# Kernel tuning notes

Measured on AMD Instinct MI355X. Metric: run time of the kernel, lower is better.

Reference implementation:

```python
import jax, jax.numpy as jnp
import numpy as np

B, S, D = 4, 2048, 512
E, K = 8, 2
MH = 4 * D      # resmlp mlp hidden
EH = 2 * D      # expert hidden
EPS = 1e-5


def setup_inputs() -> dict:
    key = jax.random.key(0)
    ks = jax.random.split(key, 16)
    s = 0.02
    return {
        "x": jax.random.normal(ks[0], (B, S, D), dtype=jnp.float32),
        "ln1_g": jnp.ones((D,), jnp.float32), "ln1_b": jnp.zeros((D,), jnp.float32),
        "w1": jax.random.normal(ks[1], (D, MH), jnp.float32) * s,
        "b1": jnp.zeros((MH,), jnp.float32),
        "w2": jax.random.normal(ks[2], (MH, D), jnp.float32) * s,
        "b2": jnp.zeros((D,), jnp.float32),
        "ln2_g": jnp.ones((D,), jnp.float32), "ln2_b": jnp.zeros((D,), jnp.float32),
        "wr": jax.random.normal(ks[3], (E, D), jnp.float32) * s,
        "ew1": jax.random.normal(ks[4], (E, D, EH), jnp.float32) * s,
        "eb1": jnp.zeros((E, EH), jnp.float32),
        "ew2": jax.random.normal(ks[5], (E, EH, D), jnp.float32) * s,
        "eb2": jnp.zeros((E, D), jnp.float32),
        "lnf_g": jnp.ones((D,), jnp.float32), "lnf_b": jnp.zeros((D,), jnp.float32),
    }


def _ln(z, g, b):
    m = z.mean(-1, keepdims=True)
    v = ((z - m) ** 2).mean(-1, keepdims=True)
    return (z - m) * jax.lax.rsqrt(v + EPS) * g + b


def reference(x, ln1_g, ln1_b, w1, b1, w2, b2, ln2_g, ln2_b,
              wr, ew1, eb1, ew2, eb2, lnf_g, lnf_b):
    # ---- ResidualMLPBlock (eval mode: dropout is identity) ----
    h = _ln(x, ln1_g, ln1_b)
    h = jax.nn.gelu(h @ w1 + b1, approximate=False) @ w2 + b2
    x = x + h
    x = _ln(x, ln2_g, ln2_b) + x
    # ---- MoE (eval: no jitter noise, aux_loss = 0) ----
    xf = x.reshape(-1, D)              # [N, D], N = B*S
    n = xf.shape[0]
    probs = jax.nn.softmax(xf @ wr.T, axis=-1)          # [N, E]
    topv, topi = jax.lax.top_k(probs, K)                # [N, K]
    topv = topv / topv.sum(-1, keepdims=True)
    # dense per-token gate per expert: sum over k of renormalized prob where idx==j
    gates = jnp.zeros((n, E), xf.dtype).at[jnp.arange(n)[:, None], topi].add(topv)
    # per-expert MLP over all tokens (masked scatter-combine via gates)
    he = jax.nn.gelu(jnp.einsum("nd,edh->enh", xf, ew1) + eb1[:, None, :],
                     approximate=False)                 # [E, N, 2D]
    ye = jnp.einsum("enh,ehd->end", he, ew2) + eb2[:, None, :]  # [E, N, D]
    out = jnp.einsum("ne,end->nd", gates, ye).reshape(B, S, D)
    # ---- final LayerNorm ----
    out = _ln(out, lnf_g, lnf_b)
    aux_loss = jnp.zeros((), x.dtype)  # eval mode
    return out, aux_loss
```

## Files before the change

kernel.cpp:

```cpp
#include <hip/hip_runtime.h>

#define NTOK 8192
#define DIM  512
#define MHID 2048
#define EHID 1024
#define NEXP 8
#define RBLK 64

using half_t = _Float16;
typedef _Float16 f16x8 __attribute__((ext_vector_type(8)));
typedef float    f32x16 __attribute__((ext_vector_type(16)));

#define MFMA32(a, b, c) __builtin_amdgcn_mfma_f32_32x32x16_f16((a), (b), (c), 0, 0, 0)

typedef const __attribute__((address_space(1))) void* gas_ptr;
typedef __attribute__((address_space(3))) void*       las_ptr;
__device__ __forceinline__ void gl16(const void* g, void* l) {
    __builtin_amdgcn_global_load_lds((gas_ptr)g, (las_ptr)l, 16, 0, 0);
}

__device__ __forceinline__ float gelu_exact(float v) {
    return 0.5f * v * (1.0f + erff(v * 0.70710678118654752f));
}

__device__ __forceinline__ float block_sum4(float v, float* red, int tid) {
#pragma unroll
    for (int off = 32; off; off >>= 1) v += __shfl_down(v, off);
    if ((tid & 63) == 0) red[tid >> 6] = v;
    __syncthreads();
    float r = red[0] + red[1] + red[2] + red[3];
    __syncthreads();
    return r;
}

__global__ __launch_bounds__(256) void ln1_split_kernel(
    const float* __restrict__ x, const float* __restrict__ g, const float* __restrict__ b,
    half_t* __restrict__ xh, half_t* __restrict__ xl, int* __restrict__ cnt)
{
    const int row = blockIdx.x, tid = threadIdx.x;
    if (row == 0) cnt[tid] = 0;
    __shared__ float red[4];
    const size_t base = (size_t)row * DIM;
    float2 v = reinterpret_cast<const float2*>(x + base)[tid];
    float mean = block_sum4(v.x + v.y, red, tid) * (1.0f / DIM);
    float d0 = v.x - mean, d1 = v.y - mean;
    float var = block_sum4(d0 * d0 + d1 * d1, red, tid) * (1.0f / DIM);
    float rstd = rsqrtf(var + 1e-5f);
    int d = tid * 2;
    float y0 = d0 * rstd * g[d]     + b[d];
    float y1 = d1 * rstd * g[d + 1] + b[d + 1];
    half_t h0 = (half_t)y0, h1 = (half_t)y1;
    xh[base + d] = h0;  xh[base + d + 1] = h1;
    xl[base + d]     = (half_t)(y0 - (float)h0);
    xl[base + d + 1] = (half_t)(y1 - (float)h1);
}

__global__ __launch_bounds__(256) void resid_ln2_kernel(
    const float* __restrict__ x, float* __restrict__ p0, const float* __restrict__ p1,
    const float* __restrict__ b2,
    const float* __restrict__ g, const float* __restrict__ b,
    half_t* __restrict__ x3h)
{
    const int row = blockIdx.x, tid = threadIdx.x;
    __shared__ float red[4];
    const size_t base = (size_t)row * DIM;
    float2 xv = reinterpret_cast<const float2*>(x + base)[tid];
    float2 h0 = reinterpret_cast<float2*>(p0 + base)[tid];
    float2 h1 = reinterpret_cast<const float2*>(p1 + base)[tid];
    float2 bb = reinterpret_cast<const float2*>(b2)[tid];
    float z0 = xv.x + h0.x + h1.x + bb.x, z1 = xv.y + h0.y + h1.y + bb.y;
    float mean = block_sum4(z0 + z1, red, tid) * (1.0f / DIM);
    float d0 = z0 - mean, d1 = z1 - mean;
    float var = block_sum4(d0 * d0 + d1 * d1, red, tid) * (1.0f / DIM);
    float rstd = rsqrtf(var + 1e-5f);
    int d = tid * 2;
    float y0 = d0 * rstd * g[d]     + b[d]     + z0;
    float y1 = d1 * rstd * g[d + 1] + b[d + 1] + z1;
    float2 o; o.x = y0; o.y = y1;
    reinterpret_cast<float2*>(p0 + base)[tid] = o;
    x3h[base + d]     = (half_t)y0;
    x3h[base + d + 1] = (half_t)y1;
}

__global__ void transpose_all_kernel(
    const float* __restrict__ w1, const float* __restrict__ w2,
    const float* __restrict__ ew1, const float* __restrict__ ew2,
    half_t* __restrict__ w1t_h, half_t* __restrict__ w1t_l,
    half_t* __restrict__ w2t_h, half_t* __restrict__ w2t_l,
    half_t* __restrict__ ew1t, half_t* __restrict__ ew2t)
{
    int bb = blockIdx.x;
    const float* in; half_t* oh; half_t* ol = (half_t*)0;
    int R, C, cx, cy; size_t mo = 0;
    if (bb < 1024)      { in = w1;  oh = w1t_h; ol = w1t_l; R = 512;  C = 2048; cx = bb & 63; cy = bb >> 6; }
    else if (bb < 2048) { bb -= 1024; in = w2;  oh = w2t_h; ol = w2t_l; R = 2048; C = 512; cx = bb & 15; cy = bb >> 4; }
    else if (bb < 6144) { bb -= 2048; int e = bb >> 9, r = bb & 511;
                          in = ew1; oh = ew1t; R = 512;  C = 1024; mo = (size_t)e * R * C; cx = r & 31; cy = r >> 5; }
    else                { bb -= 6144; int e = bb >> 9, r = bb & 511;
                          in = ew2; oh = ew2t; R = 1024; C = 512;  mo = (size_t)e * R * C; cx = r & 15; cy = r >> 4; }
    __shared__ float t[32][33];
    const int c0 = cx * 32, r0 = cy * 32;
    const int tx = threadIdx.x, ty = threadIdx.y;
    for (int i = ty; i < 32; i += 8) t[i][tx] = in[mo + (size_t)(r0 + i) * C + c0 + tx];
    __syncthreads();
    for (int i = ty; i < 32; i += 8) {
        float v = t[tx][i];
        size_t o = mo + (size_t)(c0 + i) * R + r0 + tx;
        half_t h = (half_t)v;
        oh[o] = h;
        if (ol) ol[o] = (half_t)(v - (float)h);
    }
}

template <int EPI, int NREP>
__global__ __launch_bounds__(512, 2) void gemm8_kernel(
    const half_t* __restrict__ A0, const half_t* __restrict__ A1,
    const half_t* __restrict__ B0, const half_t* __restrict__ B1,
    const float* __restrict__ bias,
    float* __restrict__ Cf0, float* __restrict__ Cf1,
    half_t* __restrict__ Ch, half_t* __restrict__ Cl,
    int Nc, int K, int Ktile)
{
    constexpr int BN    = NREP * 128;
    constexpr int LOADS = 4 + 2 * NREP;
    constexpr int TOT   = 16384 + NREP * 8192;
    __shared__ __align__(16) half_t lds[2 * TOT];

    const int m0 = blockIdx.x * 256, n0 = blockIdx.y * BN;
    const int kbeg = blockIdx.z * Ktile;
    float* Cf = blockIdx.z ? Cf1 : Cf0;
    const int tid = threadIdx.x;
    const int lane = tid & 63, wid = tid >> 6;
    const int wr = wid >> 2, wc = wid & 3;
    const int l31 = lane & 31, l5 = lane >> 5;

    const half_t* gsrc[LOADS];
    {
        const half_t* A0p = A0 + (size_t)m0 * K + kbeg;
        const half_t* A1p = A1 + (size_t)m0 * K + kbeg;
        const half_t* B0p = B0 + (size_t)n0 * K + kbeg;
        const half_t* B1p = B1 + (size_t)n0 * K + kbeg;
#pragma unroll
        for (int i = 0; i < LOADS; i++) {
            int c = tid + 512 * i;
            const half_t* base; int cm;
            if (c < 1024)                  { base = A0p; cm = c; }
            else if (c < 2048)             { base = A1p; cm = c - 1024; }
            else if (c < 2048 + NREP * 512){ base = B0p; cm = c - 2048; }
            else                           { base = B1p; cm = c - 2048 - NREP * 512; }
            int r = cm >> 2, ss = (cm & 3) ^ ((r >> 1) & 3);
            gsrc[i] = base + (size_t)r * K + ss * 8;
        }
    }

    int oa[4][2], ob[NREP][2];
#pragma unroll
    for (int m = 0; m < 4; m++)
#pragma unroll
        for (int kh = 0; kh < 2; kh++) {
            int ra = wr * 128 + m * 32 + l31;
            oa[m][kh] = ra * 32 + (((l5 + 2 * kh) ^ ((ra >> 1) & 3)) << 3);
        }
#pragma unroll
    for (int n = 0; n < NREP; n++)
#pragma unroll
        for (int kh = 0; kh < 2; kh++) {
            int rb = wc * (NREP * 32) + n * 32 + l31;
            ob[n][kh] = rb * 32 + (((l5 + 2 * kh) ^ ((rb >> 1) & 3)) << 3);
        }

    f32x16 acc[4][NREP];
#pragma unroll
    for (int m = 0; m < 4; m++)
#pragma unroll
        for (int n = 0; n < NREP; n++)
#pragma unroll
            for (int q = 0; q < 16; q++) acc[m][n][q] = 0.f;

    auto stage = [&](int bsel, int kof) {
#pragma unroll
        for (int i = 0; i < LOADS; i++)
            gl16(gsrc[i] + kof, &lds[bsel * TOT + (tid + 512 * i) * 8]);
    };
    auto compute = [&](int p) {
        const half_t* buf = &lds[p ? TOT : 0];
        __builtin_amdgcn_s_setprio(1);
#pragma unroll
        for (int kh = 0; kh < 2; kh++) {
            f16x8 ah[4], al[4], bh[NREP], bl[NREP];
#pragma unroll
            for (int m = 0; m < 4; m++) {
                ah[m] = *(const f16x8*)(buf + oa[m][kh]);
                al[m] = *(const f16x8*)(buf + 8192 + oa[m][kh]);
            }
#pragma unroll
            for (int n = 0; n < NREP; n++) {
                bh[n] = *(const f16x8*)(buf + 16384 + ob[n][kh]);
                bl[n] = *(const f16x8*)(buf + 16384 + BN * 32 + ob[n][kh]);
            }
#pragma unroll
            for (int m = 0; m < 4; m++)
#pragma unroll
                for (int n = 0; n < NREP; n++) {
                    acc[m][n] = MFMA32(ah[m], bh[n], acc[m][n]);
                    acc[m][n] = MFMA32(al[m], bh[n], acc[m][n]);
                    acc[m][n] = MFMA32(ah[m], bl[n], acc[m][n]);
                }
        }
        __builtin_amdgcn_s_setprio(0);
    };

    const int nsteps = Ktile / 32;
    stage(0, 0);
#pragma unroll 1
    for (int s = 0; s < nsteps - 1; ++s) {
        stage((s + 1) & 1, (s + 1) * 32);
        if constexpr (NREP == 2) asm volatile("s_waitcnt vmcnt(8)" ::: "memory");
        else                     asm volatile("s_waitcnt vmcnt(6)" ::: "memory");
        __builtin_amdgcn_s_barrier();
        compute(s & 1);
        __builtin_amdgcn_s_barrier();
    }
    asm volatile("s_waitcnt vmcnt(0)" ::: "memory");
    __builtin_amdgcn_s_barrier();
    compute((nsteps - 1) & 1);

    const int er = 4 * l5;
#pragma unroll
    for (int m = 0; m < 4; m++)
#pragma unroll
        for (int n = 0; n < NREP; n++) {
            int cc = n0 + wc * (NREP * 32) + n * 32 + l31;
            float bv = (EPI == 1) ? bias[cc] : 0.f;
#pragma unroll
            for (int reg = 0; reg < 16; reg++) {
                int rr = m0 + wr * 128 + m * 32 + er + 8 * (reg >> 2) + (reg & 3);
                float v = acc[m][n][reg] + bv;
                size_t o = (size_t)rr * Nc + cc;
                if (EPI == 1) {
                    float ge = gelu_exact(v);
                    half_t h = (half_t)ge;
                    Ch[o] = h;
                    Cl[o] = (half_t)(ge - (float)h);
                } else {
                    Cf[o] = v;
                }
            }
        }
}

__global__ __launch_bounds__(256) void router_kernel(
    const float* __restrict__ x3, const float* __restrict__ wrm,
    int* __restrict__ cnt, int* __restrict__ aid, float* __restrict__ gate)
{
    __shared__ float wl[NEXP][DIM];
    __shared__ int   texp[RBLK * 2];
    __shared__ float tgate[RBLK * 2];
    __shared__ int   lslot[RBLK * 2];
    __shared__ int   lcnt[NEXP], lbase[NEXP];
    const int tid = threadIdx.x;
    for (int i = tid; i < NEXP * DIM / 4; i += 256)
        reinterpret_cast<float4*>(&wl[0][0])[i] = reinterpret_cast<const float4*>(wrm)[i];
    if (tid < NEXP) lcnt[tid] = 0;
    __syncthreads();
    const int w = tid >> 6, lane = tid & 63;
#pragma unroll 1
    for (int t = 0; t < RBLK / 4; ++t) {
        const int lt = w * (RBLK / 4) + t;
        const int token = blockIdx.x * RBLK + lt;
        const float* xr = x3 + (size_t)token * DIM;
        float a[NEXP];
#pragma unroll
        for (int e = 0; e < NEXP; e++) a[e] = 0.f;
#pragma unroll
        for (int d0 = 0; d0 < DIM; d0 += 64) {
            float xv = xr[d0 + lane];
#pragma unroll
            for (int e = 0; e < NEXP; e++) a[e] += xv * wl[e][d0 + lane];
        }
#pragma unroll
        for (int e = 0; e < NEXP; e++)
#pragma unroll
            for (int off = 32; off; off >>= 1) a[e] += __shfl_xor(a[e], off);
        if (lane == 0) {
            int i1 = 0; float v1 = a[0];
#pragma unroll
            for (int e = 1; e < NEXP; e++) if (a[e] > v1) { v1 = a[e]; i1 = e; }
            int i2 = -1; float v2 = -3.4e38f;
#pragma unroll
            for (int e = 0; e < NEXP; e++) if (e != i1 && a[e] > v2) { v2 = a[e]; i2 = e; }
            float e2 = expf(v2 - v1);
            float g1 = 1.0f / (1.0f + e2);
            texp[lt * 2]      = i1; tgate[lt * 2]      = g1;
            texp[lt * 2 + 1]  = i2; tgate[lt * 2 + 1]  = 1.0f - g1;
        }
    }
    __syncthreads();
    if (tid < RBLK * 2) lslot[tid] = atomicAdd(&lcnt[texp[tid]], 1);
    __syncthreads();
    if (tid < NEXP) lbase[tid] = atomicAdd(&cnt[tid * 32], lcnt[tid]);
    __syncthreads();
    if (tid < RBLK * 2) {
        const int e = texp[tid];
        const int asg = blockIdx.x * (RBLK * 2) + tid;
        aid[e * NTOK + lbase[e] + lslot[tid]] = asg;
        gate[asg] = tgate[tid];
    }
}

__global__ __launch_bounds__(256) void egemm1_kernel(
    const half_t* __restrict__ X,
    const half_t* __restrict__ W,
    const float* __restrict__ eb1,
    const int* __restrict__ cnt, const int* __restrict__ aid,
    half_t* __restrict__ He)
{
    const int bid = blockIdx.x;
    const int e = bid >> 9, rem = bid & 511;
    const int mt = rem >> 3, nt = rem & 7;
    const int ne = cnt[e * 32];
    if (mt * 128 >= ne) return;
    __shared__ __align__(16) half_t As[2][128 * 32];
    __shared__ __align__(16) half_t Bs[2][128 * 32];
    __shared__ int rowmap[128];
    const int tid = threadIdx.x;
    if (tid < 128) {
        int slot = mt * 128 + tid;
        rowmap[tid] = (slot < ne) ? aid[e * NTOK + slot] : -1;
    }
    __syncthreads();
    const int lane = tid & 63, wid = tid >> 6;
    const int wr = wid >> 1, wc = wid & 1;
    const int c0 = tid, c1 = tid + 256;
    const int r0 = c0 >> 2, s0 = (c0 & 3) ^ ((r0 >> 1) & 3);
    const int r1 = c1 >> 2, s1 = (c1 & 3) ^ ((r1 >> 1) & 3);
    const int a0r = rowmap[r0], a1r = rowmap[r1];
    const half_t* pa0 = X + (size_t)(a0r >= 0 ? (a0r >> 1) : 0) * DIM + s0 * 8;
    const half_t* pa1 = X + (size_t)(a1r >= 0 ? (a1r >> 1) : 0) * DIM + s1 * 8;
    const half_t* pb0 = W + (size_t)e * EHID * DIM + (size_t)(nt * 128 + r0) * DIM + s0 * 8;
    const half_t* pb1 = W + (size_t)e * EHID * DIM + (size_t)(nt * 128 + r1) * DIM + s1 * 8;

    const int l31 = lane & 31, l5 = lane >> 5;
    int oa[2][2], ob[2][2];
#pragma unroll
    for (int i = 0; i < 2; i++)
#pragma unroll
        for (int kh = 0; kh < 2; kh++) {
            int ra = wr * 64 + i * 32 + l31;
            oa[i][kh] = ra * 32 + (((l5 + kh * 2) ^ ((ra >> 1) & 3)) << 3);
            int rb = wc * 64 + i * 32 + l31;
            ob[i][kh] = rb * 32 + (((l5 + kh * 2) ^ ((rb >> 1) & 3)) << 3);
        }
    f32x16 acc[2][2];
#pragma unroll
    for (int i = 0; i < 2; i++)
#pragma unroll
        for (int j = 0; j < 2; j++)
#pragma unroll
            for (int q = 0; q < 16; q++) acc[i][j][q] = 0.f;

    auto stage = [&](int bsel, int k0) {
        gl16(pa0 + k0, &As[bsel][c0 * 8]);
        gl16(pa1 + k0, &As[bsel][c1 * 8]);
        gl16(pb0 + k0, &Bs[bsel][c0 * 8]);
        gl16(pb1 + k0, &Bs[bsel][c1 * 8]);
    };
    auto compute = [&](int bsel) {
#pragma unroll
        for (int kh = 0; kh < 2; kh++) {
            f16x8 a0 = *(const f16x8*)(&As[bsel][0] + oa[0][kh]);
            f16x8 a1 = *(const f16x8*)(&As[bsel][0] + oa[1][kh]);
            f16x8 b0 = *(const f16x8*)(&Bs[bsel][0] + ob[0][kh]);
            f16x8 b1 = *(const f16x8*)(&Bs[bsel][0] + ob[1][kh]);
            acc[0][0] = MFMA32(a0, b0, acc[0][0]);
            acc[0][1] = MFMA32(a0, b1, acc[0][1]);
            acc[1][0] = MFMA32(a1, b0, acc[1][0]);
            acc[1][1] = MFMA32(a1, b1, acc[1][1]);
        }
    };

    stage(0, 0);
#pragma unroll 1
    for (int k0 = 0; k0 < DIM; k0 += 64) {
        __syncthreads();
        if (k0 + 32 < DIM) stage(1, k0 + 32);
        compute(0);
        __syncthreads();
        if (k0 + 64 < DIM) stage(0, k0 + 64);
        compute(1);
    }
    const int er = 4 * l5;
#pragma unroll
    for (int i = 0; i < 2; i++)
#pragma unroll
        for (int reg = 0; reg < 16; reg++) {
            int rloc = wr * 64 + i * 32 + er + 8 * (reg >> 2) + (reg & 3);
            int a = rowmap[rloc];
            if (a >= 0) {
#pragma unroll
                for (int j = 0; j < 2; j++) {
                    int cc = nt * 128 + wc * 64 + j * 32 + l31;
                    float v = acc[i][j][reg] + eb1[e * EHID + cc];
                    He[(size_t)a * EHID + cc] = (half_t)gelu_exact(v);
                }
            }
        }
}

__global__ __launch_bounds__(256) void egemm2_kernel(
    const half_t* __restrict__ Hin,
    const half_t* __restrict__ W,
    const float* __restrict__ eb2,
    const int* __restrict__ cnt, const int* __restrict__ aid,
    const float* __restrict__ gate,
    float* __restrict__ Ye)
{
    const int bid = blockIdx.x;
    const int e = bid >> 8, rem = bid & 255;
    const int mt = rem >> 2, nt = rem & 3;
    const int ne = cnt[e * 32];
    if (mt * 128 >= ne) return;
    __shared__ __align__(16) half_t As[2][128 * 32];
    __shared__ __align__(16) half_t Bs[2][128 * 32];
    __shared__ int rowmap[128];
    const int tid = threadIdx.x;
    if (tid < 128) {
        int slot = mt * 128 + tid;
        rowmap[tid] = (slot < ne) ? aid[e * NTOK + slot] : -1;
    }
    __syncthreads();
    const int lane = tid & 63, wid = tid >> 6;
    const int wr = wid >> 1, wc = wid & 1;
    const int l31 = lane & 31, l5 = lane >> 5;
    const int c0 = tid, c1 = tid + 256;
    const int r0 = c0 >> 2, s0 = (c0 & 3) ^ ((r0 >> 1) & 3);
    const int r1 = c1 >> 2, s1 = (c1 & 3) ^ ((r1 >> 1) & 3);
    const int a0r = rowmap[r0], a1r = rowmap[r1];
    const half_t* pa0 = Hin + (size_t)(a0r >= 0 ? a0r : 0) * EHID + s0 * 8;
    const half_t* pa1 = Hin + (size_t)(a1r >= 0 ? a1r : 0) * EHID + s1 * 8;
    const half_t* pb0 = W + (size_t)e * DIM * EHID + (size_t)(nt * 128 + r0) * EHID + s0 * 8;
    const half_t* pb1 = W + (size_t)e * DIM * EHID + (size_t)(nt * 128 + r1) * EHID + s1 * 8;

    int oa[2][2], ob[2][2];
#pragma unroll
    for (int i = 0; i < 2; i++)
#pragma unroll
        for (int kh = 0; kh < 2; kh++) {
            int ra = wr * 64 + i * 32 + l31;
            oa[i][kh] = ra * 32 + (((l5 + kh * 2) ^ ((ra >> 1) & 3)) << 3);
            int rb = wc * 64 + i * 32 + l31;
            ob[i][kh] = rb * 32 + (((l5 + kh * 2) ^ ((rb >> 1) & 3)) << 3);
        }
    f32x16 acc[2][2];
#pragma unroll
    for (int i = 0; i < 2; i++)
#pragma unroll
        for (int j = 0; j < 2; j++)
#pragma unroll
            for (int q = 0; q < 16; q++) acc[i][j][q] = 0.f;

    auto stage = [&](int bsel, int k0) {
        gl16(pa0 + k0, &As[bsel][c0 * 8]);
        gl16(pa1 + k0, &As[bsel][c1 * 8]);
        gl16(pb0 + k0, &Bs[bsel][c0 * 8]);
        gl16(pb1 + k0, &Bs[bsel][c1 * 8]);
    };
    auto compute = [&](int bsel) {
#pragma unroll
        for (int kh = 0; kh < 2; kh++) {
            f16x8 a0 = *(const f16x8*)(&As[bsel][0] + oa[0][kh]);
            f16x8 a1 = *(const f16x8*)(&As[bsel][0] + oa[1][kh]);
            f16x8 b0 = *(const f16x8*)(&Bs[bsel][0] + ob[0][kh]);
            f16x8 b1 = *(const f16x8*)(&Bs[bsel][0] + ob[1][kh]);
            acc[0][0] = MFMA32(a0, b0, acc[0][0]);
            acc[0][1] = MFMA32(a0, b1, acc[0][1]);
            acc[1][0] = MFMA32(a1, b0, acc[1][0]);
            acc[1][1] = MFMA32(a1, b1, acc[1][1]);
        }
    };

    stage(0, 0);
#pragma unroll 1
    for (int k0 = 0; k0 < EHID; k0 += 64) {
        __syncthreads();
        if (k0 + 32 < EHID) stage(1, k0 + 32);
        compute(0);
        __syncthreads();
        if (k0 + 64 < EHID) stage(0, k0 + 64);
        compute(1);
    }
    const int er = 4 * l5;
#pragma unroll
    for (int i = 0; i < 2; i++)
#pragma unroll
        for (int reg = 0; reg < 16; reg++) {
            int rloc = wr * 64 + i * 32 + er + 8 * (reg >> 2) + (reg & 3);
            int a = rowmap[rloc];
            if (a >= 0) {
                float gv = gate[a];
#pragma unroll
                for (int j = 0; j < 2; j++) {
                    int cc = nt * 128 + wc * 64 + j * 32 + l31;
                    float v = (acc[i][j][reg] + eb2[e * DIM + cc]) * gv;
                    Ye[(size_t)a * DIM + cc] = v;
                }
            }
        }
}

__global__ __launch_bounds__(256) void combine_lnf_kernel(
    const float* __restrict__ Ye, const float* __restrict__ g, const float* __restrict__ b,
    float* __restrict__ out)
{
    const int t = blockIdx.x, tid = threadIdx.x;
    __shared__ float red[4];
    float2 y0 = reinterpret_cast<const float2*>(Ye + (size_t)(2 * t) * DIM)[tid];
    float2 y1 = reinterpret_cast<const float2*>(Ye + (size_t)(2 * t + 1) * DIM)[tid];
    float z0 = y0.x + y1.x, z1 = y0.y + y1.y;
    float mean = block_sum4(z0 + z1, red, tid) * (1.0f / DIM);
    float d0 = z0 - mean, d1 = z1 - mean;
    float var = block_sum4(d0 * d0 + d1 * d1, red, tid) * (1.0f / DIM);
    float rstd = rsqrtf(var + 1e-5f);
    int d = tid * 2;
    out[(size_t)t * DIM + d]     = d0 * rstd * g[d]     + b[d];
    out[(size_t)t * DIM + d + 1] = d1 * rstd * g[d + 1] + b[d + 1];
    if (t == 0 && tid == 0) out[(size_t)NTOK * DIM] = 0.f;
}

extern "C" void kernel_launch(void* const* d_in, const int* in_sizes, int n_in,
                              void* d_out, int out_size, void* d_ws, size_t ws_size,
                              hipStream_t stream)
{
    (void)in_sizes; (void)n_in; (void)out_size; (void)ws_size;
    const float* x    = (const float*)d_in[0];
    const float* ln1g = (const float*)d_in[1];
    const float* ln1b = (const float*)d_in[2];
    const float* w1   = (const float*)d_in[3];
    const float* b1   = (const float*)d_in[4];
    const float* w2   = (const float*)d_in[5];
    const float* b2   = (const float*)d_in[6];
    const float* ln2g = (const float*)d_in[7];
    const float* ln2b = (const float*)d_in[8];
    const float* wrm  = (const float*)d_in[9];
    const float* ew1  = (const float*)d_in[10];
    const float* eb1  = (const float*)d_in[11];
    const float* ew2  = (const float*)d_in[12];
    const float* eb2  = (const float*)d_in[13];
    const float* lnfg = (const float*)d_in[14];
    const float* lnfb = (const float*)d_in[15];
    float* out = (float*)d_out;

    char* w = (char*)d_ws;
    size_t off = 0;
    auto take = [&](size_t bytes) {
        char* p = w + off;
        off += bytes;
        off = (off + 255) & ~(size_t)255;
        return p;
    };
    half_t* xh_h  = (half_t*)take((size_t)NTOK * DIM * 2);
    half_t* xh_l  = (half_t*)take((size_t)NTOK * DIM * 2);
    half_t* w1t_h = (half_t*)take((size_t)DIM * MHID * 2);
    half_t* w1t_l = (half_t*)take((size_t)DIM * MHID * 2);
    half_t* w2t_h = (half_t*)take((size_t)MHID * DIM * 2);
    half_t* w2t_l = (half_t*)take((size_t)MHID * DIM * 2);
    char*   big   = take((size_t)NTOK * MHID * 2 * 2);
    half_t* a1h   = (half_t*)big;
    half_t* a1l   = (half_t*)(big + (size_t)NTOK * MHID * 2);
    half_t* heh   = (half_t*)big;
    float*  yef   = (float*)(big + (size_t)NTOK * MHID * 2);
    float*  x3f   = (float*)take((size_t)NTOK * DIM * 4);
    half_t* x3h   = (half_t*)take((size_t)NTOK * DIM * 2);
    half_t* ew1t  = (half_t*)take((size_t)NEXP * DIM * EHID * 2);
    half_t* ew2t  = (half_t*)take((size_t)NEXP * EHID * DIM * 2);
    int*    cnt   = (int*)take(1024);
    int*    aid   = (int*)take((size_t)NEXP * NTOK * 4);
    float*  gate  = (float*)take((size_t)NTOK * 2 * 4);

    float* p0 = x3f;
    float* p1 = (float*)xh_h;

    ln1_split_kernel<<<NTOK, 256, 0, stream>>>(x, ln1g, ln1b, xh_h, xh_l, cnt);
    transpose_all_kernel<<<10240, dim3(32, 8), 0, stream>>>(
        w1, w2, ew1, ew2, w1t_h, w1t_l, w2t_h, w2t_l, ew1t, ew2t);
    gemm8_kernel<1, 2><<<dim3(NTOK / 256, MHID / 256, 1), 512, 0, stream>>>(
        xh_h, xh_l, w1t_h, w1t_l, b1, (float*)0, (float*)0, a1h, a1l, MHID, DIM, DIM);
    gemm8_kernel<0, 1><<<dim3(NTOK / 256, DIM / 128, 2), 512, 0, stream>>>(
        a1h, a1l, w2t_h, w2t_l, (const float*)0, p0, p1, (half_t*)0, (half_t*)0, DIM, MHID, MHID / 2);
    resid_ln2_kernel<<<NTOK, 256, 0, stream>>>(x, p0, p1, b2, ln2g, ln2b, x3h);
    router_kernel<<<NTOK / RBLK, 256, 0, stream>>>(x3f, wrm, cnt, aid, gate);
    egemm1_kernel<<<NEXP * (NTOK / 128) * (EHID / 128), 256, 0, stream>>>(x3h, ew1t, eb1, cnt, aid, heh);
    egemm2_kernel<<<NEXP * (NTOK / 128) * (DIM / 128), 256, 0, stream>>>(heh, ew2t, eb2, cnt, aid, gate, yef);
    combine_lnf_kernel<<<NTOK, 256, 0, stream>>>(yef, lnfg, lnfb, out);
}
```

Measured before the change: 309.1 us.

## Merge expert GEMMs into one templated kernel with 256-row tiles and waitcnt pipelining

Replaces the two expert GEMM kernels with a single templated kernel that uses 512-thread blocks and 256x128 tiles, so each weight tile is reused across twice as many routed rows. The k-loop now issues the next stage's loads before computing and waits with explicit vmcnt and raw barriers instead of two __syncthreads per pair of steps. It also raises wave priority around the MFMA section. The aim is less weight traffic and better overlap of loads with compute. The cost is more padding waste in each expert's last row tile and a higher LDS footprint per block.

```diff
diff --git a/kernel.cpp b/kernel.cpp
--- a/kernel.cpp
+++ b/kernel.cpp
@@ -308,201 +308,132 @@
     }
 }
 
-__global__ __launch_bounds__(256) void egemm1_kernel(
-    const half_t* __restrict__ X,
+template <int EG, int KDIM, int AROWSHIFT>
+__global__ __launch_bounds__(512, 2) void egemm8_kernel(
+    const half_t* __restrict__ Ain,
     const half_t* __restrict__ W,
-    const float* __restrict__ eb1,
+    const float* __restrict__ ebias,
     const int* __restrict__ cnt, const int* __restrict__ aid,
-    half_t* __restrict__ He)
-{
+    const float* __restrict__ gate,
+    half_t* __restrict__ Oh,
+    float* __restrict__ Of,
+    int Nc)
+{
+    const int ntPerE = Nc / 128;
     const int bid = blockIdx.x;
-    const int e = bid >> 9, rem = bid & 511;
-    const int mt = rem >> 3, nt = rem & 7;
-    const int ne = cnt[e * 32];
-    if (mt * 128 >= ne) return;
-    __shared__ __align__(16) half_t As[2][128 * 32];
-    __shared__ __align__(16) half_t Bs[2][128 * 32];
-    __shared__ int rowmap[128];
+    const int e   = bid / (32 * ntPerE);
+    const int rem = bid % (32 * ntPerE);
+    const int mt  = rem / ntPerE, nt = rem % ntPerE;
+    const int ne  = cnt[e * 32];
+    if (mt * 256 >= ne) return;
+
+    constexpr int TOT = 8192 + 4096;
+    __shared__ __align__(16) half_t lds[2 * TOT];
+    __shared__ int rowmap[256];
     const int tid = threadIdx.x;
-    if (tid < 128) {
-        int slot = mt * 128 + tid;
-        rowmap[tid] = (slot < ne) ? aid[e * NTOK + slot] : -1;
-    }
-    __syncthreads();
+    {
+        int slot = mt * 256 + tid;
+        if (tid < 256) rowmap[tid] = (slot < ne) ? aid[e * NTOK + slot] : -1;
+    }
+    __syncthreads();
+
     const int lane = tid & 63, wid = tid >> 6;
     const int wr = wid >> 1, wc = wid & 1;
-    const int c0 = tid, c1 = tid + 256;
-    const int r0 = c0 >> 2, s0 = (c0 & 3) ^ ((r0 >> 1) & 3);
-    const int r1 = c1 >> 2, s1 = (c1 & 3) ^ ((r1 >> 1) & 3);
-    const int a0r = rowmap[r0], a1r = rowmap[r1];
-    const half_t* pa0 = X + (size_t)(a0r >= 0 ? (a0r >> 1) : 0) * DIM + s0 * 8;
-    const half_t* pa1 = X + (size_t)(a1r >= 0 ? (a1r >> 1) : 0) * DIM + s1 * 8;
-    const half_t* pb0 = W + (size_t)e * EHID * DIM + (size_t)(nt * 128 + r0) * DIM + s0 * 8;
-    const half_t* pb1 = W + (size_t)e * EHID * DIM + (size_t)(nt * 128 + r1) * DIM + s1 * 8;
-
     const int l31 = lane & 31, l5 = lane >> 5;
+
+    const half_t* gsrc[3];
+    const half_t* Wb = W + (size_t)e * Nc * KDIM;
+#pragma unroll
+    for (int i = 0; i < 3; i++) {
+        int c = tid + 512 * i;
+        if (c < 1024) {
+            int r = c >> 2, ss = (c & 3) ^ ((r >> 1) & 3);
+            int a = rowmap[r];
+            gsrc[i] = Ain + (size_t)(a >= 0 ? (a >> AROWSHIFT) : 0) * KDIM + ss * 8;
+        } else {
+            int cb = c - 1024;
+            int r = cb >> 2, ss = (cb & 3) ^ ((r >> 1) & 3);
+            gsrc[i] = Wb + (size_t)(nt * 128 + r) * KDIM + ss * 8;
+        }
+    }
+
     int oa[2][2], ob[2][2];
 #pragma unroll
-    for (int i = 0; i < 2; i++)
+    for (int m = 0; m < 2; m++)
 #pragma unroll
         for (int kh = 0; kh < 2; kh++) {
-            int ra = wr * 64 + i * 32 + l31;
-            oa[i][kh] = ra * 32 + (((l5 + kh * 2) ^ ((ra >> 1) & 3)) << 3);
-            int rb = wc * 64 + i * 32 + l31;
-            ob[i][kh] = rb * 32 + (((l5 + kh * 2) ^ ((rb >> 1) & 3)) << 3);
-        }
+            int ra = wr * 64 + m * 32 + l31;
+            oa[m][kh] = ra * 32 + (((l5 + 2 * kh) ^ ((ra >> 1) & 3)) << 3);
+        }
+#pragma unroll
+    for (int n = 0; n < 2; n++)
+#pragma unroll
+        for (int kh = 0; kh < 2; kh++) {
+            int rb = wc * 64 + n * 32 + l31;
+            ob[n][kh] = 8192 + rb * 32 + (((l5 + 2 * kh) ^ ((rb >> 1) & 3)) << 3);
+        }
+
     f32x16 acc[2][2];
 #pragma unroll
-    for (int i = 0; i < 2; i++)
-#pragma unroll
-        for (int j = 0; j < 2; j++)
-#pragma unroll
-            for (int q = 0; q < 16; q++) acc[i][j][q] = 0.f;
-
-    auto stage = [&](int bsel, int k0) {
-        gl16(pa0 + k0, &As[bsel][c0 * 8]);
-        gl16(pa1 + k0, &As[bsel][c1 * 8]);
-        gl16(pb0 + k0, &Bs[bsel][c0 * 8]);
-        gl16(pb1 + k0, &Bs[bsel][c1 * 8]);
+    for (int m = 0; m < 2; m++)
+#pragma unroll
+        for (int n = 0; n < 2; n++)
+#pragma unroll
+            for (int q = 0; q < 16; q++) acc[m][n][q] = 0.f;
+
+    auto stage = [&](int bsel, int kof) {
+#pragma unroll
+        for (int i = 0; i < 3; i++)
+            gl16(gsrc[i] + kof, &lds[bsel * TOT + (tid + 512 * i) * 8]);
     };
-    auto compute = [&](int bsel) {
+    auto compute = [&](int p) {
+        const half_t* buf = &lds[p ? TOT : 0];
+        __builtin_amdgcn_s_setprio(1);
 #pragma unroll
         for (int kh = 0; kh < 2; kh++) {
-            f16x8 a0 = *(const f16x8*)(&As[bsel][0] + oa[0][kh]);
-            f16x8 a1 = *(const f16x8*)(&As[bsel][0] + oa[1][kh]);
-            f16x8 b0 = *(const f16x8*)(&Bs[bsel][0] + ob[0][kh]);
-            f16x8 b1 = *(const f16x8*)(&Bs[bsel][0] + ob[1][kh]);
+            f16x8 a0 = *(const f16x8*)(buf + oa[0][kh]);
+            f16x8 a1 = *(const f16x8*)(buf + oa[1][kh]);
+            f16x8 b0 = *(const f16x8*)(buf + ob[0][kh]);
+            f16x8 b1 = *(const f16x8*)(buf + ob[1][kh]);
             acc[0][0] = MFMA32(a0, b0, acc[0][0]);
             acc[0][1] = MFMA32(a0, b1, acc[0][1]);
             acc[1][0] = MFMA32(a1, b0, acc[1][0]);
             acc[1][1] = MFMA32(a1, b1, acc[1][1]);
         }
+        __builtin_amdgcn_s_setprio(0);
     };
 
+    const int nsteps = KDIM / 32;
     stage(0, 0);
 #pragma unroll 1
-    for (int k0 = 0; k0 < DIM; k0 += 64) {
-        __syncthreads();
-        if (k0 + 32 < DIM) stage(1, k0 + 32);
-        compute(0);
-        __syncthreads();
-        if (k0 + 64 < DIM) stage(0, k0 + 64);
-        compute(1);
-    }
+    for (int s = 0; s < nsteps - 1; ++s) {
+        stage((s + 1) & 1, (s + 1) * 32);
+        asm volatile("s_waitcnt vmcnt(3)" ::: "memory");
+        __builtin_amdgcn_s_barrier();
+        compute(s & 1);
+        __builtin_amdgcn_s_barrier();
+    }
+    asm volatile("s_waitcnt vmcnt(0)" ::: "memory");
+    __builtin_amdgcn_s_barrier();
+    compute((nsteps - 1) & 1);
+
     const int er = 4 * l5;
 #pragma unroll
-    for (int i = 0; i < 2; i++)
+    for (int m = 0; m < 2; m++)
 #pragma unroll
         for (int reg = 0; reg < 16; reg++) {
-            int rloc = wr * 64 + i * 32 + er + 8 * (reg >> 2) + (reg & 3);
+            int rloc = wr * 64 + m * 32 + er + 8 * (reg >> 2) + (reg & 3);
             int a = rowmap[rloc];
             if (a >= 0) {
 #pragma unroll
-                for (int j = 0; j < 2; j++) {
-                    int cc = nt * 128 + wc * 64 + j * 32 + l31;
-                    float v = acc[i][j][reg] + eb1[e * EHID + cc];
-                    He[(size_t)a * EHID + cc] = (half_t)gelu_exact(v);
-                }
-            }
-        }
-}
-
-__global__ __launch_bounds__(256) void egemm2_kernel(
-    const half_t* __restrict__ Hin,
-    const half_t* __restrict__ W,
-    const float* __restrict__ eb2,
-    const int* __restrict__ cnt, const int* __restrict__ aid,
-    const float* __restrict__ gate,
-    float* __restrict__ Ye)
-{
-    const int bid = blockIdx.x;
-    const int e = bid >> 8, rem = bid & 255;
-    const int mt = rem >> 2, nt = rem & 3;
-    const int ne = cnt[e * 32];
-    if (mt * 128 >= ne) return;
-    __shared__ __align__(16) half_t As[2][128 * 32];
-    __shared__ __align__(16) half_t Bs[2][128 * 32];
-    __shared__ int rowmap[128];
-    const int tid = threadIdx.x;
-    if (tid < 128) {
-        int slot = mt * 128 + tid;
-        rowmap[tid] = (slot < ne) ? aid[e * NTOK + slot] : -1;
-    }
-    __syncthreads();
-    const int lane = tid & 63, wid = tid >> 6;
-    const int wr = wid >> 1, wc = wid & 1;
-    const int l31 = lane & 31, l5 = lane >> 5;
-    const int c0 = tid, c1 = tid + 256;
-    const int r0 = c0 >> 2, s0 = (c0 & 3) ^ ((r0 >> 1) & 3);
-    const int r1 = c1 >> 2, s1 = (c1 & 3) ^ ((r1 >> 1) & 3);
-    const int a0r = rowmap[r0], a1r = rowmap[r1];
-    const half_t* pa0 = Hin + (size_t)(a0r >= 0 ? a0r : 0) * EHID + s0 * 8;
-    const half_t* pa1 = Hin + (size_t)(a1r >= 0 ? a1r : 0) * EHID + s1 * 8;
-    const half_t* pb0 = W + (size_t)e * DIM * EHID + (size_t)(nt * 128 + r0) * EHID + s0 * 8;
-    const half_t* pb1 = W + (size_t)e * DIM * EHID + (size_t)(nt * 128 + r1) * EHID + s1 * 8;
-
-    int oa[2][2], ob[2][2];
-#pragma unroll
-    for (int i = 0; i < 2; i++)
-#pragma unroll
-        for (int kh = 0; kh < 2; kh++) {
-            int ra = wr * 64 + i * 32 + l31;
-            oa[i][kh] = ra * 32 + (((l5 + kh * 2) ^ ((ra >> 1) & 3)) << 3);
-            int rb = wc * 64 + i * 32 + l31;
-            ob[i][kh] = rb * 32 + (((l5 + kh * 2) ^ ((rb >> 1) & 3)) << 3);
-        }
-    f32x16 acc[2][2];
-#pragma unroll
-    for (int i = 0; i < 2; i++)
-#pragma unroll
-        for (int j = 0; j < 2; j++)
-#pragma unroll
-            for (int q = 0; q < 16; q++) acc[i][j][q] = 0.f;
-
-    auto stage = [&](int bsel, int k0) {
-        gl16(pa0 + k0, &As[bsel][c0 * 8]);
-        gl16(pa1 + k0, &As[bsel][c1 * 8]);
-        gl16(pb0 + k0, &Bs[bsel][c0 * 8]);
-        gl16(pb1 + k0, &Bs[bsel][c1 * 8]);
-    };
-    auto compute = [&](int bsel) {
-#pragma unroll
-        for (int kh = 0; kh < 2; kh++) {
-            f16x8 a0 = *(const f16x8*)(&As[bsel][0] + oa[0][kh]);
-            f16x8 a1 = *(const f16x8*)(&As[bsel][0] + oa[1][kh]);
-            f16x8 b0 = *(const f16x8*)(&Bs[bsel][0] + ob[0][kh]);
-            f16x8 b1 = *(const f16x8*)(&Bs[bsel][0] + ob[1][kh]);
-            acc[0][0] = MFMA32(a0, b0, acc[0][0]);
-            acc[0][1] = MFMA32(a0, b1, acc[0][1]);
-            acc[1][0] = MFMA32(a1, b0, acc[1][0]);
-            acc[1][1] = MFMA32(a1, b1, acc[1][1]);
-        }
-    };
-
-    stage(0, 0);
-#pragma unroll 1
-    for (int k0 = 0; k0 < EHID; k0 += 64) {
-        __syncthreads();
-        if (k0 + 32 < EHID) stage(1, k0 + 32);
-        compute(0);
-        __syncthreads();
-        if (k0 + 64 < EHID) stage(0, k0 + 64);
-        compute(1);
-    }
-    const int er = 4 * l5;
-#pragma unroll
-    for (int i = 0; i < 2; i++)
-#pragma unroll
-        for (int reg = 0; reg < 16; reg++) {
-            int rloc = wr * 64 + i * 32 + er + 8 * (reg >> 2) + (reg & 3);
-            int a = rowmap[rloc];
-            if (a >= 0) {
-                float gv = gate[a];
-#pragma unroll
-                for (int j = 0; j < 2; j++) {
-                    int cc = nt * 128 + wc * 64 + j * 32 + l31;
-                    float v = (acc[i][j][reg] + eb2[e * DIM + cc]) * gv;
-                    Ye[(size_t)a * DIM + cc] = v;
+                for (int n = 0; n < 2; n++) {
+                    int cc = nt * 128 + wc * 64 + n * 32 + l31;
+                    float v = acc[m][n][reg] + ebias[e * Nc + cc];
+                    if (EG == 1) {
+                        Oh[(size_t)a * Nc + cc] = (half_t)gelu_exact(v);
+                    } else {
+                        Of[(size_t)a * Nc + cc] = v * gate[a];
+                    }
                 }
             }
         }
@@ -589,7 +520,9 @@
         a1h, a1l, w2t_h, w2t_l, (const float*)0, p0, p1, (half_t*)0, (half_t*)0, DIM, MHID, MHID / 2);
     resid_ln2_kernel<<<NTOK, 256, 0, stream>>>(x, p0, p1, b2, ln2g, ln2b, x3h);
     router_kernel<<<NTOK / RBLK, 256, 0, stream>>>(x3f, wrm, cnt, aid, gate);
-    egemm1_kernel<<<NEXP * (NTOK / 128) * (EHID / 128), 256, 0, stream>>>(x3h, ew1t, eb1, cnt, aid, heh);
-    egemm2_kernel<<<NEXP * (NTOK / 128) * (DIM / 128), 256, 0, stream>>>(heh, ew2t, eb2, cnt, aid, gate, yef);
+    egemm8_kernel<1, DIM, 1><<<NEXP * 32 * (EHID / 128), 512, 0, stream>>>(
+        x3h, ew1t, eb1, cnt, aid, (const float*)0, heh, (float*)0, EHID);
+    egemm8_kernel<2, EHID, 0><<<NEXP * 32 * (DIM / 128), 512, 0, stream>>>(
+        heh, ew2t, eb2, cnt, aid, gate, (half_t*)0, yef, DIM);
     combine_lnf_kernel<<<NTOK, 256, 0, stream>>>(yef, lnfg, lnfb, out);
 }
```

Result: no change. 306.6 us (-0.8%).
